# Kernel optimization log

Measured on AMD Instinct MI355X. Metric: run time of the kernel, lower is better.

## Reference

```python
import jax, jax.numpy as jnp
import numpy as np

NEG = -1e9


def _ln(x, g, b):
    m = x.mean(-1, keepdims=True)
    v = ((x - m) ** 2).mean(-1, keepdims=True)
    return (x - m) / jnp.sqrt(v + 1e-5) * g + b


def _block(single, pair, single_mask, pair_mask,
           pa_ln_g, pa_ln_b, pa_wqkv, pa_wg, pa_wout,
           pt_ln_g, pt_ln_b, pt_w1, pt_b1, pt_w2, pt_b2,
           sa_ln_g, sa_ln_b, sa_wq, sa_wkv, sa_wb, sa_wout,
           st_ln_g, st_ln_b, st_w1, st_b1, st_w2, st_b2):
    B, L, _, D = pair.shape
    H = sa_wb.shape[1]
    hd = D // H
    scale = 1.0 / jnp.sqrt(jnp.asarray(hd, dtype=pair.dtype))
    # ---- PairUpdate: PairAttention over L*L pseudo-tokens ----
    z = _ln(pair, pa_ln_g, pa_ln_b)                       # [B,L,L,D]
    N = L * L
    qkv = (z @ pa_wqkv).reshape(B, N, 3, H, hd)
    q = qkv[:, :, 0].transpose(0, 2, 1, 3)                # [B,H,N,hd]
    k = qkv[:, :, 1].transpose(0, 2, 1, 3)
    v = qkv[:, :, 2].transpose(0, 2, 1, 3)
    attn = jnp.einsum('bhid,bhjd->bhij', q, k) * scale    # [B,H,N,N]
    pm = pair_mask.reshape(B, 1, N)
    m = pm[:, :, :, None] * pm[:, :, None, :]             # [B,1,N,N]
    attn = jnp.where(m > 0, attn, NEG)
    attn = jax.nn.softmax(attn, axis=-1)
    out = jnp.einsum('bhij,bhjd->bhid', attn, v)          # [B,H,N,hd]
    out = out.transpose(0, 2, 1, 3).reshape(B, L, L, D)
    g = jax.nn.sigmoid(z @ pa_wg)
    out = (out @ pa_wout) * g * pair_mask[..., None]
    pair = pair + out
    t = _ln(pair, pt_ln_g, pt_ln_b)
    t = jax.nn.relu(t @ pt_w1 + pt_b1) @ pt_w2 + pt_b2
    pair = pair + t * pair_mask[..., None]
    # ---- SingleUpdate: AttentionPairBias ----
    s = _ln(single, sa_ln_g, sa_ln_b)                     # [B,L,D]
    q = (s @ sa_wq).reshape(B, L, H, hd)
    kv = (s @ sa_wkv).reshape(B, L, 2, H, hd)
    k2, v2 = kv[:, :, 0], kv[:, :, 1]
    attn = jnp.einsum('bihd,bjhd->bhij', q, k2) * scale   # [B,H,L,L]
    bias = (pair @ sa_wb).transpose(0, 3, 1, 2)           # [B,H,L,L]
    attn = attn + bias
    sm = single_mask[:, None, None, :]
    attn = jnp.where(sm > 0, attn, NEG)
    attn = jax.nn.softmax(attn, axis=-1)
    out = jnp.einsum('bhij,bjhd->bihd', attn, v2).reshape(B, L, D)
    single = single + (out @ sa_wout) * single_mask[..., None]
    # single transition
    t = _ln(single, st_ln_g, st_ln_b)
    t = jax.nn.relu(t @ st_w1 + st_b1) @ st_w2 + st_b2
    single = single + t * single_mask[..., None]
    return single, pair


def setup_inputs() -> dict:
    key = jax.random.key(0)
    B, L, D, H = 1, 64, 144, 8
    ks = iter(jax.random.split(key, 40))
    def nrm(shape, scale=0.02):
        return jax.random.normal(next(ks), shape, dtype=jnp.float32) * scale
    sm = jnp.ones((B, L), jnp.float32).at[:, L - 8:].set(0.0)
    pm = sm[:, :, None] * sm[:, None, :]
    return dict(
        single=jax.random.normal(next(ks), (B, L, D), jnp.float32),
        pair=jax.random.normal(next(ks), (B, L, L, D), jnp.float32),
        single_mask=sm,
        pair_mask=pm,
        pa_ln_g=jnp.ones((D,), jnp.float32), pa_ln_b=jnp.zeros((D,), jnp.float32),
        pa_wqkv=nrm((D, 3 * D)), pa_wg=nrm((D, D)), pa_wout=nrm((D, D)),
        pt_ln_g=jnp.ones((D,), jnp.float32), pt_ln_b=jnp.zeros((D,), jnp.float32),
        pt_w1=nrm((D, 4 * D)), pt_b1=jnp.zeros((4 * D,), jnp.float32),
        pt_w2=nrm((4 * D, D)), pt_b2=jnp.zeros((D,), jnp.float32),
        sa_ln_g=jnp.ones((D,), jnp.float32), sa_ln_b=jnp.zeros((D,), jnp.float32),
        sa_wq=nrm((D, D)), sa_wkv=nrm((D, 2 * D)), sa_wb=nrm((D, H)), sa_wout=nrm((D, D)),
        st_ln_g=jnp.ones((D,), jnp.float32), st_ln_b=jnp.zeros((D,), jnp.float32),
        st_w1=nrm((D, 4 * D)), st_b1=jnp.zeros((4 * D,), jnp.float32),
        st_w2=nrm((4 * D, D)), st_b2=jnp.zeros((D,), jnp.float32),
    )


def reference(single, pair, single_mask, pair_mask,
              pa_ln_g, pa_ln_b, pa_wqkv, pa_wg, pa_wout,
              pt_ln_g, pt_ln_b, pt_w1, pt_b1, pt_w2, pt_b2,
              sa_ln_g, sa_ln_b, sa_wq, sa_wkv, sa_wb, sa_wout,
              st_ln_g, st_ln_b, st_w1, st_b1, st_w2, st_b2):
    return _block(single, pair, single_mask, pair_mask,
                  pa_ln_g, pa_ln_b, pa_wqkv, pa_wg, pa_wout,
                  pt_ln_g, pt_ln_b, pt_w1, pt_b1, pt_w2, pt_b2,
                  sa_ln_g, sa_ln_b, sa_wq, sa_wkv, sa_wb, sa_wout,
                  st_ln_g, st_ln_b, st_w1, st_b1, st_w2, st_b2)
```

## Files before the change

kernel.cpp:

```cpp
#include <hip/hip_runtime.h>
#include <hip/hip_bf16.h>

typedef __hip_bfloat16 bf16;
typedef __attribute__((ext_vector_type(8))) short short8;
typedef __attribute__((ext_vector_type(16))) float floatx16;

__device__ __forceinline__ float tof(bf16 x){ return __bfloat162float(x); }
__device__ __forceinline__ float bflo(unsigned u){ return __uint_as_float(u<<16); }
__device__ __forceinline__ float bfhi(unsigned u){ return __uint_as_float(u & 0xFFFF0000u); }
__device__ __forceinline__ float ldT(const void* p, long i, bool isf){
  return isf ? ((const float*)p)[i] : tof(((const bf16*)p)[i]);
}
__device__ __forceinline__ void stT(void* p, long i, bool isf, float v){
  if (isf) ((float*)p)[i] = v; else ((bf16*)p)[i] = __float2bfloat16(v);
}

#define LL 64
#define DD 144
#define NN 4096
#define HH 8
#define HDIM 18
#define SCALE 0.23570226039551584f
#define LOG2E 1.4426950408889634f

__global__ void detect_dtype(const unsigned int* __restrict__ w, int* __restrict__ flag){
  *flag = (w[0] == 0x3F800000u) ? 4 : 2;
}

__global__ __launch_bounds__(256) void prep_weights(const int* __restrict__ df,
    const void* __restrict__ wqkv, const void* __restrict__ wg,
    const void* __restrict__ wout, const void* __restrict__ w1, const void* __restrict__ w2,
    const void* __restrict__ swq, const void* __restrict__ swkv,
    const void* __restrict__ swout, const void* __restrict__ sw1, const void* __restrict__ sw2,
    bf16* __restrict__ F1, bf16* __restrict__ Fout, bf16* __restrict__ Fw1,
    bf16* __restrict__ Fw2, bf16* __restrict__ Fs1, bf16* __restrict__ Wtswout,
    bf16* __restrict__ Wtst1, bf16* __restrict__ Wtst2){
  bool isf = df[0]==4;
  long t = (long)blockIdx.x*256 + threadIdx.x;
  if (t < 82944){
    int j=t&7, lane=(int)((t>>3)&63); long tk=t>>9; int ks=tk%9, tile=tk/9;
    int col=tile*32+(lane&31); int k=ks*16+(lane>>5)*8+j;
    float v = (col<432)? ldT(wqkv,(long)k*432+col,isf) : ldT(wg,(long)k*144+(col-432),isf);
    F1[t]=__float2bfloat16(v); return;
  } t -= 82944;
  if (t < 23040){
    int j=t&7, lane=(int)((t>>3)&63); long tk=t>>9; int ks=tk%9, tile=tk/9;
    int col=tile*32+(lane&31); if (col>143) col=143;
    int k=ks*16+(lane>>5)*8+j;
    Fout[t]=__float2bfloat16(ldT(wout,(long)k*144+col,isf)); return;
  } t -= 23040;
  if (t < 82944){
    int j=t&7, lane=(int)((t>>3)&63); long tk=t>>9; int ks=tk%9, tile=tk/9;
    int col=tile*32+(lane&31); int k=ks*16+(lane>>5)*8+j;
    Fw1[t]=__float2bfloat16(ldT(w1,(long)k*576+col,isf)); return;
  } t -= 82944;
  if (t < 92160){
    int j=t&7, lane=(int)((t>>3)&63); long tk=t>>9; int ks=tk%36, tile=tk/36;
    int col=tile*32+(lane&31); if (col>143) col=143;
    int k=ks*16+(lane>>5)*8+j;
    Fw2[t]=__float2bfloat16(ldT(w2,(long)k*144+col,isf)); return;
  } t -= 92160;
  if (t < 64512){
    int j=t&7, lane=(int)((t>>3)&63); long tk=t>>9; int ks=tk%9, tile=tk/9;
    int col=tile*32+(lane&31); if (col>431) col=431;
    int k=ks*16+(lane>>5)*8+j;
    float v = (col<144)? ldT(swq,(long)k*144+col,isf) : ldT(swkv,(long)k*288+(col-144),isf);
    Fs1[t]=__float2bfloat16(v); return;
  } t -= 64512;
  if (t < 20736){ int c=t/144,k=t-(long)c*144; Wtswout[t]=__float2bfloat16(ldT(swout,(long)k*144+c,isf)); return; }
  t -= 20736;
  if (t < 82944){ int c=t/144,k=t-(long)c*144; Wtst1[t]=__float2bfloat16(ldT(sw1,(long)k*576+c,isf)); return; }
  t -= 82944;
  if (t < 82944){ int c=t/576,k=t-(long)c*576; Wtst2[t]=__float2bfloat16(ldT(sw2,(long)k*144+c,isf)); return; }
}

__global__ __launch_bounds__(256) void ln_rows(const int* __restrict__ df,
    const void* __restrict__ xv,
    const void* __restrict__ gv, const void* __restrict__ bv,
    bf16* __restrict__ out){
  bool isf = (df[0]==4);
  int row = blockIdx.x*4 + (threadIdx.x>>6);
  int lane = threadIdx.x & 63;
  long base = (long)row*DD;
  float e0 = ldT(xv,base+lane,isf);
  float e1 = ldT(xv,base+lane+64,isf);
  float e2 = (lane<16) ? ldT(xv,base+lane+128,isf) : 0.f;
  float s = e0+e1+e2;
  #pragma unroll
  for (int o=32;o;o>>=1) s += __shfl_xor(s,o);
  float mean = s*(1.f/144.f);
  float d0=e0-mean, d1=e1-mean, d2=(lane<16)?(e2-mean):0.f;
  float v = d0*d0+d1*d1+d2*d2;
  #pragma unroll
  for (int o=32;o;o>>=1) v += __shfl_xor(v,o);
  float rstd = rsqrtf(v*(1.f/144.f)+1e-5f);
  out[base+lane]    = __float2bfloat16(d0*rstd*ldT(gv,lane,isf)    + ldT(bv,lane,isf));
  out[base+lane+64] = __float2bfloat16(d1*rstd*ldT(gv,lane+64,isf) + ldT(bv,lane+64,isf));
  if (lane<16)
    out[base+lane+128] = __float2bfloat16(d2*rstd*ldT(gv,lane+128,isf) + ldT(bv,lane+128,isf));
}

__global__ __launch_bounds__(256) void gemm_fused1(const int* __restrict__ df,
    const bf16* __restrict__ z, const bf16* __restrict__ F1,
    const void* __restrict__ pmask,
    bf16* __restrict__ Qb, bf16* __restrict__ Kf, bf16* __restrict__ Vf,
    bf16* __restrict__ gbuf){
  __shared__ short As[64*152];
  bool isf = df[0]==4;
  int row0 = blockIdx.y*64, col0 = blockIdx.x*64;
  int tid=threadIdx.x, lane=tid&63, l31=lane&31, w=tid>>6, wr=w>>1, wc=w&1;
  int g=(lane>>5)*8;
  for (int t=tid; t<64*72; t+=256){
    int m = t/72, dw = t%72;
    ((unsigned*)As)[m*76+dw] = ((const unsigned*)(z + (size_t)(row0+m)*144))[dw];
  }
  __syncthreads();
  int tile = blockIdx.x*2 + wc;
  const short8* wf = (const short8*)F1;
  floatx16 acc;
  #pragma unroll
  for (int i=0;i<16;i++) acc[i]=0.f;
  #pragma unroll
  for (int ks=0; ks<9; ks++){
    short8 af = *(const short8*)&As[(l31+32*wr)*152 + ks*16 + g];
    acc = __builtin_amdgcn_mfma_f32_32x32x16_bf16(af, wf[(tile*9+ks)*64+lane], acc, 0,0,0);
  }
  int col = col0 + wc*32 + l31;
  #pragma unroll
  for (int r=0;r<16;r++){
    int row = row0 + 32*wr + (r&3)+8*(r>>2)+4*(lane>>5);
    if (col < 144){
      int hh = col/18, d = col - hh*18;
      Qb[((size_t)hh*NN+row)*32 + d] = __float2bfloat16(acc[r]*(SCALE*LOG2E));
    } else if (col < 288){
      int c2 = col-144, hh = c2/18, d = c2 - hh*18;
      int f = d>>4, rem = d&15, gs = rem>>3, j = rem&7;
      Kf[((((size_t)hh*128 + (row>>5))*2 + f)*64 + gs*32 + (row&31))*8 + j]
        = __float2bfloat16(acc[r]);
    } else if (col < 432){
      int c2 = col-288, hh = c2/18, d = c2 - hh*18;
      float pm = (ldT(pmask,row,isf)>0.f)?1.f:0.f;
      int kin = row&31, f = kin>>4, k15 = kin&15;
      int gs = (k15>>2)&1, j = (k15&3) | (((k15>>3)&1)<<2);
      Vf[((((size_t)hh*128 + (row>>5))*2 + f)*64 + gs*32 + d)*8 + j]
        = __float2bfloat16(acc[r]*pm);
    } else {
      int c2 = col-432;
      float gt = 1.f/(1.f+__expf(fminf(-acc[r],30.f)));
      gbuf[(size_t)row*DD+c2] = __float2bfloat16(gt);
    }
  }
  if (blockIdx.x==0){
    for (int t=threadIdx.x; t<64*8*7; t+=256){
      int n = row0 + t/56; int rem = t%56; int hh = rem/7, dw = rem%7 + 9;
      ((unsigned*)(Qb + ((size_t)hh*NN+n)*32))[dw] = 0;
    }
    for (int t=threadIdx.x; t<64*8; t+=256){
      int n = row0 + (t>>3), hh = t&7;
      float pm = (ldT(pmask,n,isf)>0.f)?1.f:0.f;
      int kin = n&31, f = kin>>4, k15 = kin&15;
      int gs = (k15>>2)&1, j = (k15&3) | (((k15>>3)&1)<<2);
      Vf[((((size_t)hh*128 + (n>>5))*2 + f)*64 + gs*32 + 18)*8 + j] = __float2bfloat16(pm);
    }
  }
}

__global__ __launch_bounds__(256) void pair_attn_mfma(const int* __restrict__ df,
    const bf16* __restrict__ Qb, const bf16* __restrict__ Kf,
    const bf16* __restrict__ Vf, bf16* __restrict__ aob){
  __shared__ float Comb[4][32][20];
  int h = blockIdx.x >> 7, qt = blockIdx.x & 127;
  int tid = threadIdx.x;
  int w = tid >> 6, lane = tid & 63;
  int l31 = lane & 31, gsel = lane>>5;

  const unsigned* qp = (const unsigned*)(Qb + ((size_t)h*NN + qt*32 + l31)*32);
  short8 qf0, qf1;
  #pragma unroll
  for (int j=0;j<4;j++) ((unsigned*)&qf0)[j] = qp[gsel*4+j];
  #pragma unroll
  for (int j=0;j<4;j++) ((unsigned*)&qf1)[j] = qp[8+gsel*4+j];

  floatx16 o;
  #pragma unroll
  for (int i=0;i<16;i++) o[i]=0.f;

  const short8* kf8 = (const short8*)Kf + (size_t)h*16384;
  const short8* vf8 = (const short8*)Vf + (size_t)h*16384;
  int c0 = w*32;

  short8 af0 = kf8[(c0*2+0)*64 + lane];
  short8 af1 = kf8[(c0*2+1)*64 + lane];
  short8 av0 = vf8[(c0*2+0)*64 + lane];
  short8 av1 = vf8[(c0*2+1)*64 + lane];

  for (int cc=0; cc<32; cc++){
    int cn = c0 + (cc<31 ? cc+1 : 31);
    short8 naf0 = kf8[(cn*2+0)*64 + lane];
    short8 naf1 = kf8[(cn*2+1)*64 + lane];
    short8 nav0 = vf8[(cn*2+0)*64 + lane];
    short8 nav1 = vf8[(cn*2+1)*64 + lane];

    floatx16 s;
    #pragma unroll
    for (int i=0;i<16;i++) s[i]=0.f;
    s = __builtin_amdgcn_mfma_f32_32x32x16_bf16(af0, qf0, s, 0,0,0);
    s = __builtin_amdgcn_mfma_f32_32x32x16_bf16(af1, qf1, s, 0,0,0);

    short8 P1, P2;
    #pragma unroll
    for (int j=0;j<4;j++){
      unsigned e0 = __float_as_uint(__builtin_amdgcn_exp2f(s[2*j]));
      unsigned e1 = __float_as_uint(__builtin_amdgcn_exp2f(s[2*j+1]));
      ((unsigned*)&P1)[j] = (e0>>16) | (e1 & 0xFFFF0000u);
      unsigned e2 = __float_as_uint(__builtin_amdgcn_exp2f(s[8+2*j]));
      unsigned e3 = __float_as_uint(__builtin_amdgcn_exp2f(s[9+2*j]));
      ((unsigned*)&P2)[j] = (e2>>16) | (e3 & 0xFFFF0000u);
    }

    o = __builtin_amdgcn_mfma_f32_32x32x16_bf16(av0, P1, o, 0,0,0);
    o = __builtin_amdgcn_mfma_f32_32x32x16_bf16(av1, P2, o, 0,0,0);

    af0=naf0; af1=naf1; av0=nav0; av1=nav1;
  }

  #pragma unroll
  for (int r=0;r<16;r++){
    int d = (r&3) + 8*(r>>2) + 4*gsel;
    if (d < 20) Comb[w][l31][d] = o[r];
  }
  __syncthreads();
  for (int t=tid; t<32*HDIM; t+=256){
    int q = t/HDIM, d = t-q*HDIM;
    float num = Comb[0][q][d]+Comb[1][q][d]+Comb[2][q][d]+Comb[3][q][d];
    float den = Comb[0][q][18]+Comb[1][q][18]+Comb[2][q][18]+Comb[3][q][18];
    aob[(size_t)(qt*32+q)*DD + h*HDIM + d] = __float2bfloat16(num/fmaxf(den,1e-20f));
  }
}

__global__ __launch_bounds__(512) void pair_tail(const int* __restrict__ df,
    const bf16* __restrict__ aob, const bf16* __restrict__ gbuf,
    const void* __restrict__ pairv, const void* __restrict__ pmaskv,
    const bf16* __restrict__ Fout, const void* __restrict__ ptln_g, const void* __restrict__ ptln_b,
    const bf16* __restrict__ Fw1, const void* __restrict__ b1v,
    const bf16* __restrict__ Fw2, const void* __restrict__ b2v,
    const void* __restrict__ wb, void* __restrict__ outP, long outOff,
    float* __restrict__ biasb){
  __shared__ __align__(16) char smem[16384];
  float* p1  = (float*)smem;
  short* ts  = (short*)(smem + 4608);
  short* hh_ = (short*)(smem + 7040);
  float* outv = (float*)(smem + 7040);

  bool isf = df[0]==4;
  int tid=threadIdx.x, lane=tid&63, l31=lane&31, gsel=lane>>5, g=gsel*8;
  int w=tid>>6;
  int lrow = l31 & 7;
  int r0 = blockIdx.x*8;
  const short8* foutf = (const short8*)Fout;
  const short8* fw1f  = (const short8*)Fw1;
  const short8* fw2f  = (const short8*)Fw2;

  for (int t=tid; t<8*72; t+=512){
    int m=t/72, dw=t%72;
    ((unsigned*)ts)[m*76+dw] = ((const unsigned*)(aob + (size_t)(r0+m)*144))[dw];
  }
  __syncthreads();

  for (int tile=w; tile<5; tile+=8){
    int c0=tile*32;
    floatx16 acc;
    #pragma unroll
    for (int i=0;i<16;i++) acc[i]=0.f;
    #pragma unroll
    for (int ks=0; ks<9; ks++){
      short8 af = *(const short8*)&ts[lrow*152 + ks*16 + g];
      acc = __builtin_amdgcn_mfma_f32_32x32x16_bf16(af, foutf[(tile*9+ks)*64+lane], acc, 0,0,0);
    }
    if (c0+l31 < 144){
      #pragma unroll
      for (int r=0;r<16;r++){
        int row=(r&3)+8*(r>>2)+4*gsel;
        if (row<8) p1[row*144 + c0+l31] = acc[r];
      }
    }
  }
  __syncthreads();
  for (int t=tid; t<8*144; t+=512){
    int row=t/144; int col=t-row*144;
    long gidx=(long)(r0+row)*144 + col;
    float pm = (ldT(pmaskv, r0+row, isf)>0.f)?1.f:0.f;
    p1[t] = ldT(pairv,gidx,isf) + p1[t]*tof(gbuf[gidx])*pm;
  }
  __syncthreads();
  if (w < 8){
    int rr = w;
    float e0=p1[rr*144+lane], e1=p1[rr*144+lane+64], e2=(lane<16)?p1[rr*144+lane+128]:0.f;
    float s=e0+e1+e2;
    #pragma unroll
    for (int o=32;o;o>>=1) s += __shfl_xor(s,o);
    float mean=s*(1.f/144.f);
    float d0=e0-mean, d1=e1-mean, d2=(lane<16)?(e2-mean):0.f;
    float v=d0*d0+d1*d1+d2*d2;
    #pragma unroll
    for (int o=32;o;o>>=1) v += __shfl_xor(v,o);
    float rstd=rsqrtf(v*(1.f/144.f)+1e-5f);
    bf16 h0 = __float2bfloat16(d0*rstd*ldT(ptln_g,lane,isf)    + ldT(ptln_b,lane,isf));
    bf16 h1 = __float2bfloat16(d1*rstd*ldT(ptln_g,lane+64,isf) + ldT(ptln_b,lane+64,isf));
    ts[rr*152+lane]    = *reinterpret_cast<short*>(&h0);
    ts[rr*152+lane+64] = *reinterpret_cast<short*>(&h1);
    if (lane<16){
      bf16 h2 = __float2bfloat16(d2*rstd*ldT(ptln_g,lane+128,isf) + ldT(ptln_b,lane+128,isf));
      ts[rr*152+lane+128] = *reinterpret_cast<short*>(&h2);
    }
  }
  __syncthreads();
  for (int tile=w; tile<18; tile+=8){
    int c0=tile*32, colB=c0+l31;
    floatx16 acc;
    #pragma unroll
    for (int i=0;i<16;i++) acc[i]=0.f;
    #pragma unroll
    for (int ks=0; ks<9; ks++){
      short8 af = *(const short8*)&ts[lrow*152 + ks*16 + g];
      acc = __builtin_amdgcn_mfma_f32_32x32x16_bf16(af, fw1f[(tile*9+ks)*64+lane], acc, 0,0,0);
    }
    float bb = ldT(b1v,colB,isf);
    #pragma unroll
    for (int r=0;r<16;r++){
      int row=(r&3)+8*(r>>2)+4*gsel;
      if (row<8){
        bf16 hv = __float2bfloat16(fmaxf(acc[r]+bb,0.f));
        hh_[row*584 + colB] = *reinterpret_cast<short*>(&hv);
      }
    }
  }
  __syncthreads();
  floatx16 fin; int fc0 = -1;
  for (int tile=w; tile<5; tile+=8){
    int c0=tile*32;
    int colB=c0+l31; if (colB>143) colB=143;
    floatx16 acc;
    #pragma unroll
    for (int i=0;i<16;i++) acc[i]=0.f;
    #pragma unroll
    for (int ks=0; ks<36; ks++){
      short8 af = *(const short8*)&hh_[lrow*584 + ks*16 + g];
      acc = __builtin_amdgcn_mfma_f32_32x32x16_bf16(af, fw2f[(tile*36+ks)*64+lane], acc, 0,0,0);
    }
    float bb = ldT(b2v,colB,isf);
    #pragma unroll
    for (int r=0;r<16;r++){
      int row=(r&3)+8*(r>>2)+4*gsel;
      float val = 0.f;
      if (row<8){
        float pm = (ldT(pmaskv, r0+row, isf)>0.f)?1.f:0.f;
        val = p1[row*144 + colB] + (acc[r]+bb)*pm;
        if (c0+l31 < 144)
          stT(outP, outOff + (long)(r0+row)*144 + c0+l31, isf, val);
      }
      fin[r]=val;
    }
    fc0 = c0;
  }
  __syncthreads();
  if (fc0 >= 0 && fc0+l31 < 144){
    #pragma unroll
    for (int r=0;r<16;r++){
      int row=(r&3)+8*(r>>2)+4*gsel;
      if (row<8) outv[row*144 + fc0+l31] = fin[r];
    }
  }
  __syncthreads();
  {
    int n = tid>>3, hb = tid&7;
    if (n < 8){
      float acc=0.f;
      #pragma unroll 4
      for (int k=0;k<144;k++) acc += outv[n*144+k]*ldT(wb,k*8+hb,isf);
      biasb[(size_t)(r0+n)*8+hb]=acc;
    }
  }
}

__global__ __launch_bounds__(256) void gemm_s1(const int* __restrict__ df,
    const void* __restrict__ single, const void* __restrict__ g, const void* __restrict__ b,
    const bf16* __restrict__ Fs1,
    bf16* __restrict__ q_sb, bf16* __restrict__ kv_sb){
  __shared__ short As[64*152];
  bool isf = df[0]==4;
  int tid=threadIdx.x, lane=tid&63, l31=lane&31, w=tid>>6, wr=w>>1, wc=w&1;
  int gg=(lane>>5)*8;
  for (int rr=w; rr<64; rr+=4){
    long base=(long)rr*DD;
    float e0=ldT(single,base+lane,isf), e1=ldT(single,base+lane+64,isf);
    float e2=(lane<16)?ldT(single,base+lane+128,isf):0.f;
    float s=e0+e1+e2;
    #pragma unroll
    for (int o=32;o;o>>=1) s += __shfl_xor(s,o);
    float mean=s*(1.f/144.f);
    float d0=e0-mean, d1=e1-mean, d2=(lane<16)?(e2-mean):0.f;
    float v=d0*d0+d1*d1+d2*d2;
    #pragma unroll
    for (int o=32;o;o>>=1) v += __shfl_xor(v,o);
    float rstd=rsqrtf(v*(1.f/144.f)+1e-5f);
    bf16 h0=__float2bfloat16(d0*rstd*ldT(g,lane,isf)+ldT(b,lane,isf));
    bf16 h1=__float2bfloat16(d1*rstd*ldT(g,lane+64,isf)+ldT(b,lane+64,isf));
    As[rr*152+lane]=*reinterpret_cast<short*>(&h0);
    As[rr*152+lane+64]=*reinterpret_cast<short*>(&h1);
    if (lane<16){
      bf16 h2=__float2bfloat16(d2*rstd*ldT(g,lane+128,isf)+ldT(b,lane+128,isf));
      As[rr*152+lane+128]=*reinterpret_cast<short*>(&h2);
    }
  }
  __syncthreads();
  int tile = blockIdx.x*2 + wc;
  const short8* wf = (const short8*)Fs1;
  floatx16 acc;
  #pragma unroll
  for (int i=0;i<16;i++) acc[i]=0.f;
  #pragma unroll
  for (int ks=0; ks<9; ks++){
    short8 af = *(const short8*)&As[(l31+32*wr)*152 + ks*16 + gg];
    acc = __builtin_amdgcn_mfma_f32_32x32x16_bf16(af, wf[(tile*9+ks)*64+lane], acc, 0,0,0);
  }
  int col = tile*32 + l31;
  if (col < 432){
    #pragma unroll
    for (int r=0;r<16;r++){
      int row = 32*wr + (r&3)+8*(r>>2)+4*(lane>>5);
      if (col<144) q_sb[(size_t)row*DD+col] = __float2bfloat16(acc[r]);
      else kv_sb[(size_t)row*288+(col-144)] = __float2bfloat16(acc[r]);
    }
  }
}

__device__ __forceinline__ void block_ln_stats(const float* xs, float* mr){
  int tid = threadIdx.x;
  if (tid < 64){
    float e0 = xs[tid], e1 = xs[tid+64], e2 = (tid<16)?xs[tid+128]:0.f;
    float s = e0+e1+e2;
    #pragma unroll
    for (int o=32;o;o>>=1) s += __shfl_xor(s,o);
    float mean = s*(1.f/144.f);
    float d0=e0-mean, d1=e1-mean, d2=(tid<16)?(e2-mean):0.f;
    float v = d0*d0+d1*d1+d2*d2;
    #pragma unroll
    for (int o=32;o;o>>=1) v += __shfl_xor(v,o);
    if (tid==0){ mr[0]=mean; mr[1]=rsqrtf(v*(1.f/144.f)+1e-5f); }
  }
  __syncthreads();
}

__global__ __launch_bounds__(64) void single_attn(const int* __restrict__ df,
    const bf16* __restrict__ qb, const bf16* __restrict__ kvb,
    const float* __restrict__ biasb, const void* __restrict__ smask,
    bf16* __restrict__ outb){
  bool isf = df[0]==4;
  int b = blockIdx.x; int h = b>>6; int i = b&63; int j = threadIdx.x;
  __shared__ float qs[HDIM];
  __shared__ float p[64];
  if (j<HDIM) qs[j] = tof(qb[i*DD + h*HDIM + j]);
  __syncthreads();
  const bf16* kr = kvb + j*288 + h*HDIM;
  float s=0.f;
  #pragma unroll
  for (int d=0;d<HDIM;d++) s += qs[d]*tof(kr[d]);
  s = fminf(s*SCALE + biasb[(i*64+j)*8 + h], 30.f);
  float e = (ldT(smask,j,isf)>0.f) ? __expf(s) : 0.f;
  p[j]=e;
  float tot=e;
  #pragma unroll
  for (int o=32;o;o>>=1) tot += __shfl_xor(tot,o);
  tot = fmaxf(tot, 1e-20f);
  __syncthreads();
  if (j<HDIM){
    float acc=0.f;
    for (int jj=0;jj<64;jj++) acc += p[jj]*tof(kvb[jj*288 + 144 + h*HDIM + j]);
    outb[i*DD + h*HDIM + j] = __float2bfloat16(acc/tot);
  }
}

__global__ __launch_bounds__(256) void single_tail(const int* __restrict__ df,
    const void* __restrict__ single, const bf16* __restrict__ ao,
    const void* __restrict__ smask, const bf16* __restrict__ Wtswout,
    const void* __restrict__ stln_g, const void* __restrict__ stln_b,
    const bf16* __restrict__ Wtst1, const void* __restrict__ st_b1,
    const bf16* __restrict__ Wtst2, const void* __restrict__ st_b2,
    void* __restrict__ outS){
  bool isf = df[0]==4;
  __shared__ float as_[DD], s1[DD], ts[DD], hs[576], mr[2];
  int n = blockIdx.x, tid = threadIdx.x;
  if (tid<DD) as_[tid] = tof(ao[n*DD+tid]);
  __syncthreads();
  float sm = ldT(smask,n,isf);
  if (tid<DD){
    const unsigned* wr = (const unsigned*)(Wtswout + (size_t)tid*DD);
    float a=0.f;
    #pragma unroll 4
    for (int kw=0; kw<72; kw++){ unsigned u = wr[kw]; a += as_[2*kw]*bflo(u) + as_[2*kw+1]*bfhi(u); }
    s1[tid] = ldT(single,(long)n*DD+tid,isf) + a*sm;
  }
  __syncthreads();
  block_ln_stats(s1, mr);
  if (tid<DD) ts[tid] = (s1[tid]-mr[0])*mr[1]*ldT(stln_g,tid,isf) + ldT(stln_b,tid,isf);
  __syncthreads();
  for (int c=tid;c<576;c+=256){
    const unsigned* wr = (const unsigned*)(Wtst1 + (size_t)c*DD);
    float a=ldT(st_b1,c,isf);
    #pragma unroll 4
    for (int kw=0; kw<72; kw++){ unsigned u = wr[kw]; a += ts[2*kw]*bflo(u) + ts[2*kw+1]*bfhi(u); }
    hs[c]=fmaxf(a,0.f);
  }
  __syncthreads();
  if (tid<DD){
    const unsigned* wr = (const unsigned*)(Wtst2 + (size_t)tid*576);
    float a=ldT(st_b2,tid,isf);
    #pragma unroll 4
    for (int kw=0; kw<288; kw++){ unsigned u = wr[kw]; a += hs[2*kw]*bflo(u) + hs[2*kw+1]*bfhi(u); }
    stT(outS,(long)n*DD+tid,isf, s1[tid] + a*sm);
  }
}

extern "C" void kernel_launch(void* const* d_in, const int* in_sizes, int n_in,
                              void* d_out, int out_size, void* d_ws, size_t ws_size,
                              hipStream_t stream) {
  char* wsb = (char*)d_ws;
  int*   dflag = (int*)wsb;
  bf16*  F1     = (bf16*)(wsb + 16);
  bf16*  Fout   = F1 + 82944;
  bf16*  Fw1    = Fout + 23040;
  bf16*  Fw2    = Fw1 + 82944;
  bf16*  Fs1    = Fw2 + 92160;
  bf16*  Wtswout= Fs1 + 64512;
  bf16*  Wtst1  = Wtswout + 20736;
  bf16*  Wtst2  = Wtst1 + 82944;
  bf16*  Qb   = Wtst2 + 82944;
  bf16*  Kf   = Qb + (size_t)HH*NN*32;
  bf16*  Vf   = Kf + (size_t)HH*131072;
  bf16*  gbuf = Vf + (size_t)HH*131072;
  bf16*  z    = gbuf + (size_t)NN*DD;
  bf16*  aob  = z + (size_t)NN*DD;
  float* biasb= (float*)(aob + (size_t)NN*DD);
  bf16*  q_sb = (bf16*)(biasb + NN*8);
  bf16*  kv_sb= q_sb + LL*DD;
  bf16*  ao_sb= kv_sb + LL*288;

  const long OUTP_OFF = (long)LL*DD;

  detect_dtype<<<1,1,0,stream>>>((const unsigned int*)d_in[2], dflag);
  prep_weights<<<2079,256,0,stream>>>(dflag, d_in[6], d_in[7], d_in[8], d_in[11], d_in[13],
      d_in[17], d_in[18], d_in[20], d_in[23], d_in[25],
      F1, Fout, Fw1, Fw2, Fs1, Wtswout, Wtst1, Wtst2);

  ln_rows<<<NN/4,256,0,stream>>>(dflag, d_in[1], d_in[4], d_in[5], z);
  gemm_fused1<<<dim3(9,64),256,0,stream>>>(dflag, z, F1, d_in[3], Qb, Kf, Vf, gbuf);
  pair_attn_mfma<<<1024,256,0,stream>>>(dflag, Qb, Kf, Vf, aob);
  pair_tail<<<512,512,0,stream>>>(dflag, aob, gbuf, d_in[1], d_in[3],
                                  Fout, d_in[9], d_in[10], Fw1, d_in[12],
                                  Fw2, d_in[14], d_in[19], d_out, OUTP_OFF, biasb);

  gemm_s1<<<dim3(7,1),256,0,stream>>>(dflag, d_in[0], d_in[15], d_in[16], Fs1, q_sb, kv_sb);
  single_attn<<<HH*LL,64,0,stream>>>(dflag, q_sb, kv_sb, biasb, d_in[2], ao_sb);
  single_tail<<<LL,256,0,stream>>>(dflag, d_in[0], ao_sb, d_in[2], Wtswout,
                                   d_in[21], d_in[22], Wtst1, d_in[24], Wtst2, d_in[26],
                                   d_out);
  (void)in_sizes; (void)n_in; (void)out_size; (void)ws_size;
}
```

Before: 237.7 us.

## Split pair attention keys across two blocks and merge partials in pair_tail

Pair attention now uses a split-K layout. Each query tile is handled by two blocks, each covering half of the key chunks. Each block writes unnormalized fp32 numerator and denominator partials to a workspace buffer, and pair_tail sums the two halves and normalizes while loading its input tile. This doubles the grid to raise occupancy and parallelism on the dominant attention kernel, at the cost of extra fp32 partial traffic and more work in the pair_tail prologue. Separately, the single-thread dtype-detection kernel is folded into prep_weights to save one launch.

Result: no change. 239.2 us (+0.6%).

```diff
diff --git a/kernel.cpp b/kernel.cpp
--- a/kernel.cpp
+++ b/kernel.cpp
@@ -23,11 +23,8 @@
 #define SCALE 0.23570226039551584f
 #define LOG2E 1.4426950408889634f
 
-__global__ void detect_dtype(const unsigned int* __restrict__ w, int* __restrict__ flag){
-  *flag = (w[0] == 0x3F800000u) ? 4 : 2;
-}
-
-__global__ __launch_bounds__(256) void prep_weights(const int* __restrict__ df,
+__global__ __launch_bounds__(256) void prep_weights(const unsigned* __restrict__ smaskw,
+    int* __restrict__ dflag,
     const void* __restrict__ wqkv, const void* __restrict__ wg,
     const void* __restrict__ wout, const void* __restrict__ w1, const void* __restrict__ w2,
     const void* __restrict__ swq, const void* __restrict__ swkv,
@@ -35,7 +32,8 @@
     bf16* __restrict__ F1, bf16* __restrict__ Fout, bf16* __restrict__ Fw1,
     bf16* __restrict__ Fw2, bf16* __restrict__ Fs1, bf16* __restrict__ Wtswout,
     bf16* __restrict__ Wtst1, bf16* __restrict__ Wtst2){
-  bool isf = df[0]==4;
+  bool isf = (smaskw[0] == 0x3F800000u);
+  if (blockIdx.x==0 && threadIdx.x==0) dflag[0] = isf ? 4 : 2;
   long t = (long)blockIdx.x*256 + threadIdx.x;
   if (t < 82944){
     int j=t&7, lane=(int)((t>>3)&63); long tk=t>>9; int ks=tk%9, tile=tk/9;
@@ -167,9 +165,10 @@
 
 __global__ __launch_bounds__(256) void pair_attn_mfma(const int* __restrict__ df,
     const bf16* __restrict__ Qb, const bf16* __restrict__ Kf,
-    const bf16* __restrict__ Vf, bf16* __restrict__ aob){
+    const bf16* __restrict__ Vf, float* __restrict__ part){
   __shared__ float Comb[4][32][20];
-  int h = blockIdx.x >> 7, qt = blockIdx.x & 127;
+  int bx = blockIdx.x;
+  int h = bx >> 8, rem = bx & 255, qt = rem >> 1, kspl = rem & 1;
   int tid = threadIdx.x;
   int w = tid >> 6, lane = tid & 63;
   int l31 = lane & 31, gsel = lane>>5;
@@ -187,15 +186,15 @@
 
   const short8* kf8 = (const short8*)Kf + (size_t)h*16384;
   const short8* vf8 = (const short8*)Vf + (size_t)h*16384;
-  int c0 = w*32;
+  int c0 = kspl*64 + w*16;
 
   short8 af0 = kf8[(c0*2+0)*64 + lane];
   short8 af1 = kf8[(c0*2+1)*64 + lane];
   short8 av0 = vf8[(c0*2+0)*64 + lane];
   short8 av1 = vf8[(c0*2+1)*64 + lane];
 
-  for (int cc=0; cc<32; cc++){
-    int cn = c0 + (cc<31 ? cc+1 : 31);
+  for (int cc=0; cc<16; cc++){
+    int cn = c0 + (cc<15 ? cc+1 : 15);
     short8 naf0 = kf8[(cn*2+0)*64 + lane];
     short8 naf1 = kf8[(cn*2+1)*64 + lane];
     short8 nav0 = vf8[(cn*2+0)*64 + lane];
@@ -230,16 +229,15 @@
     if (d < 20) Comb[w][l31][d] = o[r];
   }
   __syncthreads();
-  for (int t=tid; t<32*HDIM; t+=256){
-    int q = t/HDIM, d = t-q*HDIM;
-    float num = Comb[0][q][d]+Comb[1][q][d]+Comb[2][q][d]+Comb[3][q][d];
-    float den = Comb[0][q][18]+Comb[1][q][18]+Comb[2][q][18]+Comb[3][q][18];
-    aob[(size_t)(qt*32+q)*DD + h*HDIM + d] = __float2bfloat16(num/fmaxf(den,1e-20f));
+  float* pb = part + ((size_t)(kspl*8+h)*NN + qt*32)*20;
+  for (int t=tid; t<32*20; t+=256){
+    int q = t/20, d = t-q*20;
+    pb[q*20+d] = Comb[0][q][d]+Comb[1][q][d]+Comb[2][q][d]+Comb[3][q][d];
   }
 }
 
 __global__ __launch_bounds__(512) void pair_tail(const int* __restrict__ df,
-    const bf16* __restrict__ aob, const bf16* __restrict__ gbuf,
+    const float* __restrict__ part, const bf16* __restrict__ gbuf,
     const void* __restrict__ pairv, const void* __restrict__ pmaskv,
     const bf16* __restrict__ Fout, const void* __restrict__ ptln_g, const void* __restrict__ ptln_b,
     const bf16* __restrict__ Fw1, const void* __restrict__ b1v,
@@ -261,9 +259,16 @@
   const short8* fw1f  = (const short8*)Fw1;
   const short8* fw2f  = (const short8*)Fw2;
 
-  for (int t=tid; t<8*72; t+=512){
-    int m=t/72, dw=t%72;
-    ((unsigned*)ts)[m*76+dw] = ((const unsigned*)(aob + (size_t)(r0+m)*144))[dw];
+  for (int t=tid; t<8*144; t+=512){
+    int m=t/144, col=t-m*144;
+    int hh=col/18, d=col-hh*18;
+    long n = r0 + m;
+    const float* p0 = part + ((size_t)hh*NN + n)*20;
+    const float* p1v = part + ((size_t)(8+hh)*NN + n)*20;
+    float num = p0[d] + p1v[d];
+    float den = fmaxf(p0[18] + p1v[18], 1e-20f);
+    bf16 v = __float2bfloat16(num/den);
+    ts[m*152+col] = *reinterpret_cast<short*>(&v);
   }
   __syncthreads();
 
@@ -540,23 +545,23 @@
   bf16*  Vf   = Kf + (size_t)HH*131072;
   bf16*  gbuf = Vf + (size_t)HH*131072;
   bf16*  z    = gbuf + (size_t)NN*DD;
-  bf16*  aob  = z + (size_t)NN*DD;
-  float* biasb= (float*)(aob + (size_t)NN*DD);
+  float* part = (float*)(z + (size_t)NN*DD);
+  float* biasb= part + (size_t)16*NN*20;
   bf16*  q_sb = (bf16*)(biasb + NN*8);
   bf16*  kv_sb= q_sb + LL*DD;
   bf16*  ao_sb= kv_sb + LL*288;
 
   const long OUTP_OFF = (long)LL*DD;
 
-  detect_dtype<<<1,1,0,stream>>>((const unsigned int*)d_in[2], dflag);
-  prep_weights<<<2079,256,0,stream>>>(dflag, d_in[6], d_in[7], d_in[8], d_in[11], d_in[13],
+  prep_weights<<<2079,256,0,stream>>>((const unsigned*)d_in[2], dflag,
+      d_in[6], d_in[7], d_in[8], d_in[11], d_in[13],
       d_in[17], d_in[18], d_in[20], d_in[23], d_in[25],
       F1, Fout, Fw1, Fw2, Fs1, Wtswout, Wtst1, Wtst2);
 
   ln_rows<<<NN/4,256,0,stream>>>(dflag, d_in[1], d_in[4], d_in[5], z);
   gemm_fused1<<<dim3(9,64),256,0,stream>>>(dflag, z, F1, d_in[3], Qb, Kf, Vf, gbuf);
-  pair_attn_mfma<<<1024,256,0,stream>>>(dflag, Qb, Kf, Vf, aob);
-  pair_tail<<<512,512,0,stream>>>(dflag, aob, gbuf, d_in[1], d_in[3],
+  pair_attn_mfma<<<2048,256,0,stream>>>(dflag, Qb, Kf, Vf, part);
+  pair_tail<<<512,512,0,stream>>>(dflag, part, gbuf, d_in[1], d_in[3],
                                   Fout, d_in[9], d_in[10], Fw1, d_in[12],
                                   Fw2, d_in[14], d_in[19], d_out, OUTP_OFF, biasb);
 
```

## Fuse single attention into single tail and fold dtype detection into weight prep

Applied to the files above, without the earlier changes.

Removes the separate single_attn kernel by computing the single-row pair-biased attention inside single_tail. Each block stages the full K/V matrix and its bias row in shared memory. The detect_dtype launch is also dropped, with prep_weights reading the mask word itself and writing the flag. This removes two kernel launches and a global round-trip for the attention output. In exchange, every one of the 64 blocks reloads the whole KV buffer (about 37KB) into shared memory.

Result: no change. 238.5 us, median of 2 (+0.3%).

```diff
diff --git a/kernel.cpp b/kernel.cpp
--- a/kernel.cpp
+++ b/kernel.cpp
@@ -23,11 +23,8 @@
 #define SCALE 0.23570226039551584f
 #define LOG2E 1.4426950408889634f
 
-__global__ void detect_dtype(const unsigned int* __restrict__ w, int* __restrict__ flag){
-  *flag = (w[0] == 0x3F800000u) ? 4 : 2;
-}
-
-__global__ __launch_bounds__(256) void prep_weights(const int* __restrict__ df,
+__global__ __launch_bounds__(256) void prep_weights(const unsigned* __restrict__ smaskw,
+    int* __restrict__ dflag,
     const void* __restrict__ wqkv, const void* __restrict__ wg,
     const void* __restrict__ wout, const void* __restrict__ w1, const void* __restrict__ w2,
     const void* __restrict__ swq, const void* __restrict__ swkv,
@@ -35,7 +32,8 @@
     bf16* __restrict__ F1, bf16* __restrict__ Fout, bf16* __restrict__ Fw1,
     bf16* __restrict__ Fw2, bf16* __restrict__ Fs1, bf16* __restrict__ Wtswout,
     bf16* __restrict__ Wtst1, bf16* __restrict__ Wtst2){
-  bool isf = df[0]==4;
+  bool isf = (smaskw[0] == 0x3F800000u);
+  if (blockIdx.x==0 && threadIdx.x==0) dflag[0] = isf ? 4 : 2;
   long t = (long)blockIdx.x*256 + threadIdx.x;
   if (t < 82944){
     int j=t&7, lane=(int)((t>>3)&63); long tk=t>>9; int ks=tk%9, tile=tk/9;
@@ -435,63 +433,58 @@
   }
 }
 
-__device__ __forceinline__ void block_ln_stats(const float* xs, float* mr){
-  int tid = threadIdx.x;
-  if (tid < 64){
-    float e0 = xs[tid], e1 = xs[tid+64], e2 = (tid<16)?xs[tid+128]:0.f;
-    float s = e0+e1+e2;
-    #pragma unroll
-    for (int o=32;o;o>>=1) s += __shfl_xor(s,o);
-    float mean = s*(1.f/144.f);
-    float d0=e0-mean, d1=e1-mean, d2=(tid<16)?(e2-mean):0.f;
-    float v = d0*d0+d1*d1+d2*d2;
-    #pragma unroll
-    for (int o=32;o;o>>=1) v += __shfl_xor(v,o);
-    if (tid==0){ mr[0]=mean; mr[1]=rsqrtf(v*(1.f/144.f)+1e-5f); }
-  }
-  __syncthreads();
-}
-
-__global__ __launch_bounds__(64) void single_attn(const int* __restrict__ df,
-    const bf16* __restrict__ qb, const bf16* __restrict__ kvb,
-    const float* __restrict__ biasb, const void* __restrict__ smask,
-    bf16* __restrict__ outb){
-  bool isf = df[0]==4;
-  int b = blockIdx.x; int h = b>>6; int i = b&63; int j = threadIdx.x;
-  __shared__ float qs[HDIM];
-  __shared__ float p[64];
-  if (j<HDIM) qs[j] = tof(qb[i*DD + h*HDIM + j]);
-  __syncthreads();
-  const bf16* kr = kvb + j*288 + h*HDIM;
-  float s=0.f;
-  #pragma unroll
-  for (int d=0;d<HDIM;d++) s += qs[d]*tof(kr[d]);
-  s = fminf(s*SCALE + biasb[(i*64+j)*8 + h], 30.f);
-  float e = (ldT(smask,j,isf)>0.f) ? __expf(s) : 0.f;
-  p[j]=e;
-  float tot=e;
-  #pragma unroll
-  for (int o=32;o;o>>=1) tot += __shfl_xor(tot,o);
-  tot = fmaxf(tot, 1e-20f);
-  __syncthreads();
-  if (j<HDIM){
-    float acc=0.f;
-    for (int jj=0;jj<64;jj++) acc += p[jj]*tof(kvb[jj*288 + 144 + h*HDIM + j]);
-    outb[i*DD + h*HDIM + j] = __float2bfloat16(acc/tot);
-  }
-}
-
 __global__ __launch_bounds__(256) void single_tail(const int* __restrict__ df,
-    const void* __restrict__ single, const bf16* __restrict__ ao,
+    const void* __restrict__ single, const bf16* __restrict__ q_sb,
+    const bf16* __restrict__ kv_sb, const float* __restrict__ biasb,
     const void* __restrict__ smask, const bf16* __restrict__ Wtswout,
     const void* __restrict__ stln_g, const void* __restrict__ stln_b,
     const bf16* __restrict__ Wtst1, const void* __restrict__ st_b1,
     const bf16* __restrict__ Wtst2, const void* __restrict__ st_b2,
     void* __restrict__ outS){
   bool isf = df[0]==4;
-  __shared__ float as_[DD], s1[DD], ts[DD], hs[576], mr[2];
+  __shared__ short kvs[64*288];
+  __shared__ float pexp[8][64];
+  __shared__ float tot[8];
+  __shared__ float bb[512];
+  __shared__ float qs[DD], as_[DD], s1[DD], tss[DD], hs[576];
   int n = blockIdx.x, tid = threadIdx.x;
-  if (tid<DD) as_[tid] = tof(ao[n*DD+tid]);
+  for (int t=tid; t<64*144; t+=256)
+    ((unsigned*)kvs)[t] = ((const unsigned*)kv_sb)[t];
+  if (tid<DD) qs[tid] = tof(q_sb[(size_t)n*DD+tid]);
+  for (int t=tid; t<512; t+=256) bb[t] = biasb[(size_t)n*512 + t];
+  __syncthreads();
+  #pragma unroll
+  for (int pp=0; pp<2; pp++){
+    int pi = tid + pp*256;
+    int h = pi>>6, j = pi&63;
+    const short* kr = &kvs[j*288 + h*HDIM];
+    float s=0.f;
+    #pragma unroll
+    for (int d=0;d<HDIM;d++){
+      unsigned u = ((unsigned)(unsigned short)kr[d])<<16;
+      s += qs[h*HDIM+d]*__uint_as_float(u);
+    }
+    s = fminf(s*SCALE + bb[j*8+h], 30.f);
+    pexp[h][j] = (ldT(smask,j,isf)>0.f) ? __expf(s) : 0.f;
+  }
+  __syncthreads();
+  if (tid<8){
+    float t2=0.f;
+    #pragma unroll 4
+    for (int j=0;j<64;j++) t2 += pexp[tid][j];
+    tot[tid] = fmaxf(t2,1e-20f);
+  }
+  __syncthreads();
+  if (tid<DD){
+    int h = tid/HDIM, d = tid - h*HDIM;
+    float acc=0.f;
+    #pragma unroll 4
+    for (int j=0;j<64;j++){
+      unsigned u = ((unsigned)(unsigned short)kvs[j*288 + 144 + h*HDIM + d])<<16;
+      acc += pexp[h][j]*__uint_as_float(u);
+    }
+    as_[tid] = acc/tot[h];
+  }
   __syncthreads();
   float sm = ldT(smask,n,isf);
   if (tid<DD){
@@ -502,14 +495,27 @@
     s1[tid] = ldT(single,(long)n*DD+tid,isf) + a*sm;
   }
   __syncthreads();
-  block_ln_stats(s1, mr);
-  if (tid<DD) ts[tid] = (s1[tid]-mr[0])*mr[1]*ldT(stln_g,tid,isf) + ldT(stln_b,tid,isf);
+  __shared__ float mr[2];
+  if (tid < 64){
+    float e0 = s1[tid], e1 = s1[tid+64], e2 = (tid<16)?s1[tid+128]:0.f;
+    float s = e0+e1+e2;
+    #pragma unroll
+    for (int o=32;o;o>>=1) s += __shfl_xor(s,o);
+    float mean = s*(1.f/144.f);
+    float d0=e0-mean, d1=e1-mean, d2=(tid<16)?(e2-mean):0.f;
+    float v = d0*d0+d1*d1+d2*d2;
+    #pragma unroll
+    for (int o=32;o;o>>=1) v += __shfl_xor(v,o);
+    if (tid==0){ mr[0]=mean; mr[1]=rsqrtf(v*(1.f/144.f)+1e-5f); }
+  }
+  __syncthreads();
+  if (tid<DD) tss[tid] = (s1[tid]-mr[0])*mr[1]*ldT(stln_g,tid,isf) + ldT(stln_b,tid,isf);
   __syncthreads();
   for (int c=tid;c<576;c+=256){
     const unsigned* wr = (const unsigned*)(Wtst1 + (size_t)c*DD);
     float a=ldT(st_b1,c,isf);
     #pragma unroll 4
-    for (int kw=0; kw<72; kw++){ unsigned u = wr[kw]; a += ts[2*kw]*bflo(u) + ts[2*kw+1]*bfhi(u); }
+    for (int kw=0; kw<72; kw++){ unsigned u = wr[kw]; a += tss[2*kw]*bflo(u) + tss[2*kw+1]*bfhi(u); }
     hs[c]=fmaxf(a,0.f);
   }
   __syncthreads();
@@ -544,12 +550,11 @@
   float* biasb= (float*)(aob + (size_t)NN*DD);
   bf16*  q_sb = (bf16*)(biasb + NN*8);
   bf16*  kv_sb= q_sb + LL*DD;
-  bf16*  ao_sb= kv_sb + LL*288;
 
   const long OUTP_OFF = (long)LL*DD;
 
-  detect_dtype<<<1,1,0,stream>>>((const unsigned int*)d_in[2], dflag);
-  prep_weights<<<2079,256,0,stream>>>(dflag, d_in[6], d_in[7], d_in[8], d_in[11], d_in[13],
+  prep_weights<<<2079,256,0,stream>>>((const unsigned*)d_in[2], dflag,
+      d_in[6], d_in[7], d_in[8], d_in[11], d_in[13],
       d_in[17], d_in[18], d_in[20], d_in[23], d_in[25],
       F1, Fout, Fw1, Fw2, Fs1, Wtswout, Wtst1, Wtst2);
 
@@ -561,9 +566,8 @@
                                   Fw2, d_in[14], d_in[19], d_out, OUTP_OFF, biasb);
 
   gemm_s1<<<dim3(7,1),256,0,stream>>>(dflag, d_in[0], d_in[15], d_in[16], Fs1, q_sb, kv_sb);
-  single_attn<<<HH*LL,64,0,stream>>>(dflag, q_sb, kv_sb, biasb, d_in[2], ao_sb);
-  single_tail<<<LL,256,0,stream>>>(dflag, d_in[0], ao_sb, d_in[2], Wtswout,
-                                   d_in[21], d_in[22], Wtst1, d_in[24], Wtst2, d_in[26],
-                                   d_out);
+  single_tail<<<LL,256,0,stream>>>(dflag, d_in[0], q_sb, kv_sb, biasb, d_in[2],
+                                   Wtswout, d_in[21], d_in[22], Wtst1, d_in[24],
+                                   Wtst2, d_in[26], d_out);
   (void)in_sizes; (void)n_in; (void)out_size; (void)ws_size;
 }
```
